# Performance work log

Hardware: AMD Instinct MI355X
Metric: run time of the kernel (lower is better)

## Reference

```python
import math
import jax, jax.numpy as jnp
import numpy as np

S, H, D = 2048, 16, 128

def setup_inputs() -> dict:
    key = jax.random.key(0)
    kq, kk, kv = jax.random.split(key, 3)
    Q = jax.random.normal(kq, (S, H, D), dtype=jnp.float32)
    K = jax.random.normal(kk, (S, H, D), dtype=jnp.float32)
    V = jax.random.normal(kv, (S, H, D), dtype=jnp.float32)
    return {"Q": Q, "K": K, "V": V}

def reference(Q, K, V):
    s, h, d = Q.shape
    # scores[i,h,j] = sum_d Q[i,h,d] * K[j,h,d]  (torch einsum 'ijk,kjl->ijl' with K.T)
    scores = jnp.einsum('ihd,jhd->ihj', Q, K) / np.float32(math.sqrt(d))
    # causal mask: y -= triu(inf, 1) broadcast over heads -> -inf above diagonal
    causal = jnp.triu(jnp.ones((s, s), dtype=bool), k=1)  # [S, S]
    scores = jnp.where(causal[:, None, :], -jnp.inf, scores)
    attn = jax.nn.softmax(scores, axis=2)  # softmax over keys (dim 2)
    # out[i,h,d] = sum_j attn[i,h,j] * V[j,h,d]
    return jnp.einsum('ihj,jhd->ihd', attn, V)
```

## Files before the change

### kernel.cpp

```cpp
#include <hip/hip_runtime.h>
#include <hip/hip_bf16.h>

#define S_LEN 2048
#define NH 16
#define HD 128
#define KBLK 128
#define SM_BOUND 14.0f

typedef short short8 __attribute__((ext_vector_type(8)));
typedef float f32x4 __attribute__((ext_vector_type(4)));

#define MFMA32(a, b, c) __builtin_amdgcn_mfma_f32_16x16x32_bf16(a, b, c, 0, 0, 0)

__device__ __forceinline__ ushort f2bf(float f) {
  union { float f; unsigned u; } v; v.f = f;
  unsigned u = v.u;
  return (ushort)((u + 0x7fffu + ((u >> 16) & 1u)) >> 16);
}

#define GLDS(gp, lp)                                                      \
  __builtin_amdgcn_global_load_lds(                                       \
      (const __attribute__((address_space(1))) void*)(gp),                \
      (__attribute__((address_space(3))) void*)(lp), 16, 0, 0)

__global__ __launch_bounds__(256)
void prep(const float* __restrict__ Kg, const float* __restrict__ Vg,
          ushort* __restrict__ Kb, ushort* __restrict__ Vb) {
  __shared__ ushort lt[64 * HD];
  const int tid = threadIdx.x;
  const int h = blockIdx.x & 15;
  const int j0 = (blockIdx.x >> 4) * 64;

#pragma unroll
  for (int it = 0; it < 8; ++it) {
    int flat = it * 256 + tid;
    int r = flat >> 5, d4 = (flat & 31) * 4;
    float4 v = *(const float4*)(Kg + ((size_t)(j0 + r) * NH + h) * HD + d4);
    ushort4 b;
    b.x = f2bf(v.x); b.y = f2bf(v.y); b.z = f2bf(v.z); b.w = f2bf(v.w);
    *(ushort4*)(Kb + ((size_t)h * S_LEN + j0 + r) * HD + d4) = b;
  }
#pragma unroll
  for (int it = 0; it < 8; ++it) {
    int flat = it * 256 + tid;
    int r = flat >> 5, d4 = (flat & 31) * 4;
    float4 v = *(const float4*)(Vg + ((size_t)(j0 + r) * NH + h) * HD + d4);
    ushort4 b;
    b.x = f2bf(v.x); b.y = f2bf(v.y); b.z = f2bf(v.z); b.w = f2bf(v.w);
    *(ushort4*)(&lt[r * 128 + (d4 ^ ((r & 7) << 3))]) = b;
  }
  __syncthreads();
  const int d = tid >> 1, half = tid & 1;
  ushort vals[32];
#pragma unroll
  for (int j = 0; j < 32; ++j) {
    int jjj = half * 32 + j;
    vals[j] = lt[jjj * 128 + (d ^ ((jjj & 7) << 3))];
  }
  ushort* dst = Vb + ((size_t)h * HD + d) * S_LEN + j0 + half * 32;
#pragma unroll
  for (int q = 0; q < 4; ++q) {
    short8 w;
#pragma unroll
    for (int e = 0; e < 8; ++e) w[e] = (short)vals[q * 8 + e];
    *(short8*)(dst + q * 8) = w;
  }
}

__global__ __launch_bounds__(512, 2)
void attn_fwd8(const float* __restrict__ Qg, const ushort* __restrict__ Kb,
               const ushort* __restrict__ Vb, float* __restrict__ Og) {
  __shared__ ushort lds_k[2][KBLK * HD];
  __shared__ ushort lds_vt[HD * KBLK];
  __shared__ ushort lds_p[64 * KBLK];
  __shared__ float  lsc[2][4][2][16];

  const int tid = threadIdx.x;
  const int l   = tid & 63;
  const int wv  = tid >> 6;
  const int qf  = wv >> 2;
  const int kh  = wv & 3;
  const int dh  = wv & 3;
  const int lr  = l & 15;
  const int lg  = l >> 4;

  const int bid = blockIdx.x;
  const int h   = bid & 15;
  const int jj  = bid >> 4;
  const int qtA = 31 - jj;
  const int qbA = qtA * 64, qbB = jj * 64;
  const int nchA = (qtA >> 1) + 1;
  const int nch  = 17;

  const ushort* khp = Kb + (size_t)h * S_LEN * HD;
  const ushort* vhp = Vb + (size_t)h * HD * S_LEN;

  int koff[4], voff[4];
#pragma unroll
  for (int i = 0; i < 4; ++i) {
    int Dg = i * 512 + tid;
    int r = Dg >> 4, gp = Dg & 15;
    koff[i] = r * 128 + ((gp ^ (r & 7)) << 3);
    voff[i] = r * S_LEN + ((gp ^ (r & 7)) << 3);
  }
  auto stageK = [&](int buf, int kc) {
    const ushort* kbase = khp + (size_t)kc * (KBLK * HD);
#pragma unroll
    for (int i = 0; i < 4; ++i)
      GLDS(kbase + koff[i], &lds_k[buf][(i * 512 + tid) * 8]);
  };
  auto stageV = [&](int kc) {
    const ushort* vbase = vhp + (size_t)kc * KBLK;
#pragma unroll
    for (int i = 0; i < 4; ++i)
      GLDS(vbase + voff[i], &lds_vt[(i * 512 + tid) * 8]);
  };
  auto kc_of = [&](int g) { return (g < nchA) ? g : (g - nchA); };

  const float scale = 0.08838834764831845f;
  short8 qfrA[2][4], qfrB[2][4];
  auto loadQ = [&](short8 (&dst)[2][4], int qb) {
#pragma unroll
    for (int qc = 0; qc < 2; ++qc) {
      const float* qsrc = Qg + ((size_t)(qb + qf * 32 + qc * 16 + lr) * NH + h) * HD;
#pragma unroll
      for (int dk = 0; dk < 4; ++dk) {
        float4 a = *(const float4*)(qsrc + dk * 32 + lg * 8);
        float4 b2 = *(const float4*)(qsrc + dk * 32 + lg * 8 + 4);
        short8 f;
        f[0] = (short)f2bf(a.x * scale);  f[1] = (short)f2bf(a.y * scale);
        f[2] = (short)f2bf(a.z * scale);  f[3] = (short)f2bf(a.w * scale);
        f[4] = (short)f2bf(b2.x * scale); f[5] = (short)f2bf(b2.y * scale);
        f[6] = (short)f2bf(b2.z * scale); f[7] = (short)f2bf(b2.w * scale);
        dst[qc][dk] = f;
      }
    }
  };
  loadQ(qfrA, qbA);
  loadQ(qfrB, qbB);

  f32x4 oacc[2][2];
#pragma unroll
  for (int qc = 0; qc < 2; ++qc)
#pragma unroll
    for (int dt = 0; dt < 2; ++dt) oacc[qc][dt] = (f32x4){0.f, 0.f, 0.f, 0.f};
  float l_run[2] = {0.f, 0.f};

  auto epilogue = [&](int qb) {
    float t0 = l_run[0], t1 = l_run[1];
    t0 += __shfl_xor(t0, 16, 64); t0 += __shfl_xor(t0, 32, 64);
    t1 += __shfl_xor(t1, 16, 64); t1 += __shfl_xor(t1, 32, 64);
    if (lg == 0) { lsc[qf][kh][0][lr] = t0; lsc[qf][kh][1][lr] = t1; }
    asm volatile("s_waitcnt lgkmcnt(0)" ::: "memory");
    asm volatile("s_barrier" ::: "memory");
    float inv[2][4];
#pragma unroll
    for (int qc = 0; qc < 2; ++qc)
#pragma unroll
      for (int i = 0; i < 4; ++i) {
        int q15 = lg * 4 + i;
        float sl = (lsc[qf][0][qc][q15] + lsc[qf][1][qc][q15]) +
                   (lsc[qf][2][qc][q15] + lsc[qf][3][qc][q15]);
        inv[qc][i] = 1.0f / sl;
      }
#pragma unroll
    for (int qc = 0; qc < 2; ++qc)
#pragma unroll
      for (int dt = 0; dt < 2; ++dt)
#pragma unroll
        for (int i = 0; i < 4; ++i) {
          int qg = qb + qf * 32 + qc * 16 + lg * 4 + i;
          Og[((size_t)qg * NH + h) * HD + dh * 32 + dt * 16 + lr] =
              oacc[qc][dt][i] * inv[qc][i];
        }
    asm volatile("s_barrier" ::: "memory");
  };

  stageK(0, 0);
  stageV(0);
  stageK(1, (nchA > 1) ? 1 : 0);
  asm volatile("s_waitcnt vmcnt(0)" ::: "memory");
  __syncthreads();

  for (int g = 0; g < nch; ++g) {
    if (g + 1 < nch) { asm volatile("s_waitcnt vmcnt(4)" ::: "memory"); }
    else             { asm volatile("s_waitcnt vmcnt(0)" ::: "memory"); }
    asm volatile("s_barrier" ::: "memory");

    const int b = g & 1;
    const ushort* lk = lds_k[b];
    const bool tB = (g >= nchA);
    const int kc = kc_of(g);
    const int qb = tB ? qbB : qbA;
    const bool diag = (g == nchA - 1) || (g == nch - 1);

    f32x4 s00 = (f32x4){0.f, 0.f, 0.f, 0.f};
    f32x4 s01 = (f32x4){0.f, 0.f, 0.f, 0.f};
    f32x4 s10 = (f32x4){0.f, 0.f, 0.f, 0.f};
    f32x4 s11 = (f32x4){0.f, 0.f, 0.f, 0.f};
    const int krow0 = kh * 32 + lr;
    const int krow1 = krow0 + 16;
    __builtin_amdgcn_s_setprio(1);
    if (!tB) {
#pragma unroll
      for (int dk = 0; dk < 4; ++dk) {
        short8 kf0 = *(const short8*)&lk[krow0 * 128 + ((dk * 32 + lg * 8) ^ ((krow0 & 7) << 3))];
        short8 kf1 = *(const short8*)&lk[krow1 * 128 + ((dk * 32 + lg * 8) ^ ((krow1 & 7) << 3))];
        s00 = MFMA32(kf0, qfrA[0][dk], s00);
        s01 = MFMA32(kf0, qfrA[1][dk], s01);
        s10 = MFMA32(kf1, qfrA[0][dk], s10);
        s11 = MFMA32(kf1, qfrA[1][dk], s11);
      }
    } else {
#pragma unroll
      for (int dk = 0; dk < 4; ++dk) {
        short8 kf0 = *(const short8*)&lk[krow0 * 128 + ((dk * 32 + lg * 8) ^ ((krow0 & 7) << 3))];
        short8 kf1 = *(const short8*)&lk[krow1 * 128 + ((dk * 32 + lg * 8) ^ ((krow1 & 7) << 3))];
        s00 = MFMA32(kf0, qfrB[0][dk], s00);
        s01 = MFMA32(kf0, qfrB[1][dk], s01);
        s10 = MFMA32(kf1, qfrB[0][dk], s10);
        s11 = MFMA32(kf1, qfrB[1][dk], s11);
      }
    }
    __builtin_amdgcn_s_setprio(0);

    float p[2][2][4];
    if (diag) {
#pragma unroll
      for (int qc = 0; qc < 2; ++qc) {
        int qg = qb + qf * 32 + qc * 16 + lr;
#pragma unroll
        for (int i = 0; i < 4; ++i) {
          int kg0 = kc * 128 + kh * 32 + lg * 4 + i;
          float e;
          e = __expf((qc ? s01 : s00)[i] - SM_BOUND);
          p[0][qc][i] = (kg0 > qg) ? 0.f : e;
          e = __expf((qc ? s11 : s10)[i] - SM_BOUND);
          p[1][qc][i] = (kg0 + 16 > qg) ? 0.f : e;
        }
      }
    } else {
#pragma unroll
      for (int i = 0; i < 4; ++i) {
        p[0][0][i] = __expf(s00[i] - SM_BOUND);
        p[0][1][i] = __expf(s01[i] - SM_BOUND);
        p[1][0][i] = __expf(s10[i] - SM_BOUND);
        p[1][1][i] = __expf(s11[i] - SM_BOUND);
      }
    }
#pragma unroll
    for (int qc = 0; qc < 2; ++qc)
      l_run[qc] += ((p[0][qc][0] + p[0][qc][1]) + (p[0][qc][2] + p[0][qc][3])) +
                   ((p[1][qc][0] + p[1][qc][1]) + (p[1][qc][2] + p[1][qc][3]));

#pragma unroll
    for (int qc = 0; qc < 2; ++qc) {
      int q = qf * 32 + qc * 16 + lr;
      int sw = (q & 7) << 3;
#pragma unroll
      for (int kcc = 0; kcc < 2; ++kcc) {
        int kb = kh * 32 + kcc * 16 + lg * 4;
        unsigned w;
        asm("v_cvt_pk_bf16_f32 %0, %1, %2" : "=v"(w) : "v"(p[kcc][qc][0]), "v"(p[kcc][qc][1]));
        *(unsigned*)&lds_p[q * 128 + ((((kb) >> 3 << 3) ^ sw) + (kb & 7))] = w;
        asm("v_cvt_pk_bf16_f32 %0, %1, %2" : "=v"(w) : "v"(p[kcc][qc][2]), "v"(p[kcc][qc][3]));
        *(unsigned*)&lds_p[q * 128 + ((((kb + 2) >> 3 << 3) ^ sw) + ((kb + 2) & 7))] = w;
      }
    }
    asm volatile("s_waitcnt lgkmcnt(0)" ::: "memory");
    asm volatile("s_barrier" ::: "memory");
    __builtin_amdgcn_sched_barrier(0);

    short8 pa0[4], pa1[4];
    {
      int q0 = qf * 32 + lr, q1 = q0 + 16;
#pragma unroll
      for (int ks = 0; ks < 4; ++ks) {
        pa0[ks] = *(const short8*)&lds_p[q0 * 128 + (((ks * 4 + lg) ^ (q0 & 7)) << 3)];
        pa1[ks] = *(const short8*)&lds_p[q1 * 128 + (((ks * 4 + lg) ^ (q1 & 7)) << 3)];
      }
    }
    __builtin_amdgcn_s_setprio(1);
#pragma unroll
    for (int dt = 0; dt < 2; ++dt) {
      int d = dh * 32 + dt * 16 + lr;
#pragma unroll
      for (int ks = 0; ks < 4; ++ks) {
        short8 vf = *(const short8*)&lds_vt[d * 128 + (((ks * 4 + lg) ^ (d & 7)) << 3)];
        oacc[0][dt] = MFMA32(pa0[ks], vf, oacc[0][dt]);
        oacc[1][dt] = MFMA32(pa1[ks], vf, oacc[1][dt]);
      }
    }
    __builtin_amdgcn_s_setprio(0);

    asm volatile("s_barrier" ::: "memory");
    if (g + 1 < nch) stageV(kc_of(g + 1));
    if (g + 2 < nch) stageK(b, kc_of(g + 2));

    if (g == nchA - 1) {
      epilogue(qbA);
#pragma unroll
      for (int qc = 0; qc < 2; ++qc)
#pragma unroll
        for (int dt = 0; dt < 2; ++dt) oacc[qc][dt] = (f32x4){0.f, 0.f, 0.f, 0.f};
      l_run[0] = 0.f; l_run[1] = 0.f;
    }
  }
  epilogue(qbB);
}

__global__ __launch_bounds__(256, 2)
void attn_fwd_fb(const float* __restrict__ Qg, const float* __restrict__ Kg,
                 const float* __restrict__ Vg, float* __restrict__ Og) {
  __shared__ ushort lds_k[64 * HD];
  __shared__ ushort lds_vt[HD * 64];
  __shared__ ushort lds_p[4][16 * 64];

  const int tid = threadIdx.x;
  const int l  = tid & 63;
  const int wv = tid >> 6;
  const int lr = l & 15;
  const int lg = l >> 4;

  const int bid = blockIdx.x;
  const int h  = bid & 15;
  const int qi = bid >> 4;
  const int qt = (qi < 16) ? (31 - 2 * qi) : (2 * (qi - 16));
  const int qbase = qt * 64;

  short8 qf[4];
  {
    const float* qsrc = Qg + ((size_t)(qbase + wv * 16 + lr) * NH + h) * HD;
#pragma unroll
    for (int dk = 0; dk < 4; ++dk) {
      float4 a = *(const float4*)(qsrc + dk * 32 + lg * 8);
      float4 b = *(const float4*)(qsrc + dk * 32 + lg * 8 + 4);
      short8 f;
      f[0] = (short)f2bf(a.x); f[1] = (short)f2bf(a.y);
      f[2] = (short)f2bf(a.z); f[3] = (short)f2bf(a.w);
      f[4] = (short)f2bf(b.x); f[5] = (short)f2bf(b.y);
      f[6] = (short)f2bf(b.z); f[7] = (short)f2bf(b.w);
      qf[dk] = f;
    }
  }

  f32x4 oacc[8];
#pragma unroll
  for (int dt = 0; dt < 8; ++dt) oacc[dt] = (f32x4){0.f, 0.f, 0.f, 0.f};
  float l_run[4] = {0.f, 0.f, 0.f, 0.f};

  const float scale = 0.08838834764831845f;
  const int nch = qt + 1;

  for (int c = 0; c < nch; ++c) {
    const int k0 = c * 64;
    __syncthreads();
#pragma unroll
    for (int it = 0; it < 8; ++it) {
      int flat = (it * 256 + tid) * 4;
      int r = flat >> 7, d = flat & 127;
      float4 v = *(const float4*)(Kg + ((size_t)(k0 + r) * NH + h) * HD + d);
      int idx = (r * 128 + d) ^ ((r & 7) << 3);
      ushort4 b4;
      b4.x = f2bf(v.x); b4.y = f2bf(v.y); b4.z = f2bf(v.z); b4.w = f2bf(v.w);
      *(ushort4*)&lds_k[idx] = b4;
    }
#pragma unroll
    for (int it = 0; it < 8; ++it) {
      int d0 = wv * 32 + it * 4;
      float4 v = *(const float4*)(Vg + ((size_t)(k0 + l) * NH + h) * HD + d0);
      lds_vt[((d0 + 0) * 64 + l) ^ (((d0 + 0) & 7) << 3)] = f2bf(v.x);
      lds_vt[((d0 + 1) * 64 + l) ^ (((d0 + 1) & 7) << 3)] = f2bf(v.y);
      lds_vt[((d0 + 2) * 64 + l) ^ (((d0 + 2) & 7) << 3)] = f2bf(v.z);
      lds_vt[((d0 + 3) * 64 + l) ^ (((d0 + 3) & 7) << 3)] = f2bf(v.w);
    }
    __syncthreads();

    f32x4 sacc[4];
#pragma unroll
    for (int kc = 0; kc < 4; ++kc) {
      sacc[kc] = (f32x4){0.f, 0.f, 0.f, 0.f};
#pragma unroll
      for (int dk = 0; dk < 4; ++dk) {
        int row = kc * 16 + lr;
        int idx = (row * 128 + dk * 32 + lg * 8) ^ ((row & 7) << 3);
        short8 kf = *(const short8*)&lds_k[idx];
        sacc[kc] = MFMA32(qf[dk], kf, sacc[kc]);
      }
    }

    float p[4][4];
    if (c == qt) {
#pragma unroll
      for (int i = 0; i < 4; ++i) {
        int qg = qbase + wv * 16 + lg * 4 + i;
#pragma unroll
        for (int kc = 0; kc < 4; ++kc) {
          float e = __expf(sacc[kc][i] * scale - SM_BOUND);
          p[kc][i] = (k0 + kc * 16 + lr > qg) ? 0.f : e;
        }
      }
    } else {
#pragma unroll
      for (int i = 0; i < 4; ++i)
#pragma unroll
        for (int kc = 0; kc < 4; ++kc)
          p[kc][i] = __expf(sacc[kc][i] * scale - SM_BOUND);
    }
#pragma unroll
    for (int i = 0; i < 4; ++i)
      l_run[i] += (p[0][i] + p[1][i]) + (p[2][i] + p[3][i]);

#pragma unroll
    for (int kc = 0; kc < 4; ++kc)
#pragma unroll
      for (int i = 0; i < 4; ++i) {
        int row = lg * 4 + i, col = kc * 16 + lr;
        lds_p[wv][(row * 64 + col) ^ ((row & 7) << 3)] = f2bf(p[kc][i]);
      }
    asm volatile("s_waitcnt lgkmcnt(0)" ::: "memory");
    __builtin_amdgcn_sched_barrier(0);

    short8 pa[2];
#pragma unroll
    for (int ks = 0; ks < 2; ++ks) {
      int idx = (lr * 64 + ks * 32 + lg * 8) ^ ((lr & 7) << 3);
      pa[ks] = *(const short8*)&lds_p[wv][idx];
    }

#pragma unroll
    for (int dt = 0; dt < 8; ++dt) {
#pragma unroll
      for (int ks = 0; ks < 2; ++ks) {
        int d = dt * 16 + lr;
        int idx = (d * 64 + ks * 32 + lg * 8) ^ ((d & 7) << 3);
        short8 vf = *(const short8*)&lds_vt[idx];
        oacc[dt] = MFMA32(pa[ks], vf, oacc[dt]);
      }
    }
  }

#pragma unroll
  for (int mk = 1; mk <= 8; mk <<= 1)
#pragma unroll
    for (int i = 0; i < 4; ++i)
      l_run[i] += __shfl_xor(l_run[i], mk, 64);
  float inv[4];
#pragma unroll
  for (int i = 0; i < 4; ++i) inv[i] = 1.0f / l_run[i];
#pragma unroll
  for (int dt = 0; dt < 8; ++dt)
#pragma unroll
    for (int i = 0; i < 4; ++i) {
      int qg = qbase + wv * 16 + lg * 4 + i;
      Og[((size_t)qg * NH + h) * HD + dt * 16 + lr] = oacc[dt][i] * inv[i];
    }
}

extern "C" void kernel_launch(void* const* d_in, const int* in_sizes, int n_in,
                              void* d_out, int out_size, void* d_ws, size_t ws_size,
                              hipStream_t stream) {
  (void)in_sizes; (void)n_in; (void)out_size;
  const float* Q = (const float*)d_in[0];
  const float* K = (const float*)d_in[1];
  const float* V = (const float*)d_in[2];
  float* O = (float*)d_out;

  const size_t elems = (size_t)S_LEN * NH * HD;
  const size_t need = 2 * elems * sizeof(ushort);
  if (ws_size >= need) {
    ushort* Kb = (ushort*)d_ws;
    ushort* Vb = Kb + elems;
    prep<<<dim3(512), dim3(256), 0, stream>>>(K, V, Kb, Vb);
    attn_fwd8<<<dim3(256), dim3(512), 0, stream>>>(Q, Kb, Vb, O);
  } else {
    attn_fwd_fb<<<dim3(512), dim3(256), 0, stream>>>(Q, K, V, O);
  }
}
```

Baseline: 60.14 us.

## Double workgroup size to 16 waves, halving per-wave key and head-dim slices

The attention kernel now runs 1024 threads (16 waves) per block instead of 512. Each wave handles 16 key rows of the S tile and 16 head-dim columns of the output rather than 32, so per-wave MFMA work, accumulator registers and staging loads are halved. The aim is more latency hiding and wave-level parallelism per CU with the same 256-block grid. In exchange, the 16 waves take part in every barrier, the row-sum reduction sums over 8 partials, and the launch bound of 4 blocks per CU may be unreachable given the LDS footprint.

New measurement: 127.4 us. 112% more time.

```diff
diff --git a/kernel.cpp b/kernel.cpp
--- a/kernel.cpp
+++ b/kernel.cpp
@@ -67,20 +67,20 @@
   }
 }
 
-__global__ __launch_bounds__(512, 2)
-void attn_fwd8(const float* __restrict__ Qg, const ushort* __restrict__ Kb,
+__global__ __launch_bounds__(1024, 4)
+void attn_fwd9(const float* __restrict__ Qg, const ushort* __restrict__ Kb,
                const ushort* __restrict__ Vb, float* __restrict__ Og) {
   __shared__ ushort lds_k[2][KBLK * HD];
   __shared__ ushort lds_vt[HD * KBLK];
   __shared__ ushort lds_p[64 * KBLK];
-  __shared__ float  lsc[2][4][2][16];
+  __shared__ float  lsc[2][8][2][16];
 
   const int tid = threadIdx.x;
   const int l   = tid & 63;
   const int wv  = tid >> 6;
-  const int qf  = wv >> 2;
-  const int kh  = wv & 3;
-  const int dh  = wv & 3;
+  const int qf  = wv >> 3;
+  const int kh  = wv & 7;
+  const int dh  = wv & 7;
   const int lr  = l & 15;
   const int lg  = l >> 4;
 
@@ -95,10 +95,10 @@
   const ushort* khp = Kb + (size_t)h * S_LEN * HD;
   const ushort* vhp = Vb + (size_t)h * HD * S_LEN;
 
-  int koff[4], voff[4];
-#pragma unroll
-  for (int i = 0; i < 4; ++i) {
-    int Dg = i * 512 + tid;
+  int koff[2], voff[2];
+#pragma unroll
+  for (int i = 0; i < 2; ++i) {
+    int Dg = i * 1024 + tid;
     int r = Dg >> 4, gp = Dg & 15;
     koff[i] = r * 128 + ((gp ^ (r & 7)) << 3);
     voff[i] = r * S_LEN + ((gp ^ (r & 7)) << 3);
@@ -106,14 +106,14 @@
   auto stageK = [&](int buf, int kc) {
     const ushort* kbase = khp + (size_t)kc * (KBLK * HD);
 #pragma unroll
-    for (int i = 0; i < 4; ++i)
-      GLDS(kbase + koff[i], &lds_k[buf][(i * 512 + tid) * 8]);
+    for (int i = 0; i < 2; ++i)
+      GLDS(kbase + koff[i], &lds_k[buf][(i * 1024 + tid) * 8]);
   };
   auto stageV = [&](int kc) {
     const ushort* vbase = vhp + (size_t)kc * KBLK;
 #pragma unroll
-    for (int i = 0; i < 4; ++i)
-      GLDS(vbase + voff[i], &lds_vt[(i * 512 + tid) * 8]);
+    for (int i = 0; i < 2; ++i)
+      GLDS(vbase + voff[i], &lds_vt[(i * 1024 + tid) * 8]);
   };
   auto kc_of = [&](int g) { return (g < nchA) ? g : (g - nchA); };
 
@@ -139,11 +139,9 @@
   loadQ(qfrA, qbA);
   loadQ(qfrB, qbB);
 
-  f32x4 oacc[2][2];
-#pragma unroll
-  for (int qc = 0; qc < 2; ++qc)
-#pragma unroll
-    for (int dt = 0; dt < 2; ++dt) oacc[qc][dt] = (f32x4){0.f, 0.f, 0.f, 0.f};
+  f32x4 oacc[2];
+  oacc[0] = (f32x4){0.f, 0.f, 0.f, 0.f};
+  oacc[1] = (f32x4){0.f, 0.f, 0.f, 0.f};
   float l_run[2] = {0.f, 0.f};
 
   auto epilogue = [&](int qb) {
@@ -159,31 +157,30 @@
 #pragma unroll
       for (int i = 0; i < 4; ++i) {
         int q15 = lg * 4 + i;
-        float sl = (lsc[qf][0][qc][q15] + lsc[qf][1][qc][q15]) +
-                   (lsc[qf][2][qc][q15] + lsc[qf][3][qc][q15]);
+        float sl = ((lsc[qf][0][qc][q15] + lsc[qf][1][qc][q15]) +
+                    (lsc[qf][2][qc][q15] + lsc[qf][3][qc][q15])) +
+                   ((lsc[qf][4][qc][q15] + lsc[qf][5][qc][q15]) +
+                    (lsc[qf][6][qc][q15] + lsc[qf][7][qc][q15]));
         inv[qc][i] = 1.0f / sl;
       }
 #pragma unroll
     for (int qc = 0; qc < 2; ++qc)
 #pragma unroll
-      for (int dt = 0; dt < 2; ++dt)
-#pragma unroll
-        for (int i = 0; i < 4; ++i) {
-          int qg = qb + qf * 32 + qc * 16 + lg * 4 + i;
-          Og[((size_t)qg * NH + h) * HD + dh * 32 + dt * 16 + lr] =
-              oacc[qc][dt][i] * inv[qc][i];
-        }
+      for (int i = 0; i < 4; ++i) {
+        int qg = qb + qf * 32 + qc * 16 + lg * 4 + i;
+        Og[((size_t)qg * NH + h) * HD + dh * 16 + lr] = oacc[qc][i] * inv[qc][i];
+      }
     asm volatile("s_barrier" ::: "memory");
   };
 
   stageK(0, 0);
   stageV(0);
-  stageK(1, (nchA > 1) ? 1 : 0);
+  stageK(1, 1);
   asm volatile("s_waitcnt vmcnt(0)" ::: "memory");
   __syncthreads();
 
   for (int g = 0; g < nch; ++g) {
-    if (g + 1 < nch) { asm volatile("s_waitcnt vmcnt(4)" ::: "memory"); }
+    if (g + 1 < nch) { asm volatile("s_waitcnt vmcnt(2)" ::: "memory"); }
     else             { asm volatile("s_waitcnt vmcnt(0)" ::: "memory"); }
     asm volatile("s_barrier" ::: "memory");
 
@@ -194,78 +191,59 @@
     const int qb = tB ? qbB : qbA;
     const bool diag = (g == nchA - 1) || (g == nch - 1);
 
-    f32x4 s00 = (f32x4){0.f, 0.f, 0.f, 0.f};
-    f32x4 s01 = (f32x4){0.f, 0.f, 0.f, 0.f};
-    f32x4 s10 = (f32x4){0.f, 0.f, 0.f, 0.f};
-    f32x4 s11 = (f32x4){0.f, 0.f, 0.f, 0.f};
-    const int krow0 = kh * 32 + lr;
-    const int krow1 = krow0 + 16;
+    f32x4 s0 = (f32x4){0.f, 0.f, 0.f, 0.f};
+    f32x4 s1 = (f32x4){0.f, 0.f, 0.f, 0.f};
+    const int krow = kh * 16 + lr;
     __builtin_amdgcn_s_setprio(1);
     if (!tB) {
 #pragma unroll
       for (int dk = 0; dk < 4; ++dk) {
-        short8 kf0 = *(const short8*)&lk[krow0 * 128 + ((dk * 32 + lg * 8) ^ ((krow0 & 7) << 3))];
-        short8 kf1 = *(const short8*)&lk[krow1 * 128 + ((dk * 32 + lg * 8) ^ ((krow1 & 7) << 3))];
-        s00 = MFMA32(kf0, qfrA[0][dk], s00);
-        s01 = MFMA32(kf0, qfrA[1][dk], s01);
-        s10 = MFMA32(kf1, qfrA[0][dk], s10);
-        s11 = MFMA32(kf1, qfrA[1][dk], s11);
+        short8 kf = *(const short8*)&lk[krow * 128 + ((dk * 32 + lg * 8) ^ ((krow & 7) << 3))];
+        s0 = MFMA32(kf, qfrA[0][dk], s0);
+        s1 = MFMA32(kf, qfrA[1][dk], s1);
       }
     } else {
 #pragma unroll
       for (int dk = 0; dk < 4; ++dk) {
-        short8 kf0 = *(const short8*)&lk[krow0 * 128 + ((dk * 32 + lg * 8) ^ ((krow0 & 7) << 3))];
-        short8 kf1 = *(const short8*)&lk[krow1 * 128 + ((dk * 32 + lg * 8) ^ ((krow1 & 7) << 3))];
-        s00 = MFMA32(kf0, qfrB[0][dk], s00);
-        s01 = MFMA32(kf0, qfrB[1][dk], s01);
-        s10 = MFMA32(kf1, qfrB[0][dk], s10);
-        s11 = MFMA32(kf1, qfrB[1][dk], s11);
+        short8 kf = *(const short8*)&lk[krow * 128 + ((dk * 32 + lg * 8) ^ ((krow & 7) << 3))];
+        s0 = MFMA32(kf, qfrB[0][dk], s0);
+        s1 = MFMA32(kf, qfrB[1][dk], s1);
       }
     }
     __builtin_amdgcn_s_setprio(0);
 
-    float p[2][2][4];
+    float p[2][4];
     if (diag) {
 #pragma unroll
       for (int qc = 0; qc < 2; ++qc) {
         int qg = qb + qf * 32 + qc * 16 + lr;
 #pragma unroll
         for (int i = 0; i < 4; ++i) {
-          int kg0 = kc * 128 + kh * 32 + lg * 4 + i;
-          float e;
-          e = __expf((qc ? s01 : s00)[i] - SM_BOUND);
-          p[0][qc][i] = (kg0 > qg) ? 0.f : e;
-          e = __expf((qc ? s11 : s10)[i] - SM_BOUND);
-          p[1][qc][i] = (kg0 + 16 > qg) ? 0.f : e;
+          int kg = kc * 128 + kh * 16 + lg * 4 + i;
+          float e = __expf((qc ? s1 : s0)[i] - SM_BOUND);
+          p[qc][i] = (kg > qg) ? 0.f : e;
         }
       }
     } else {
 #pragma unroll
       for (int i = 0; i < 4; ++i) {
-        p[0][0][i] = __expf(s00[i] - SM_BOUND);
-        p[0][1][i] = __expf(s01[i] - SM_BOUND);
-        p[1][0][i] = __expf(s10[i] - SM_BOUND);
-        p[1][1][i] = __expf(s11[i] - SM_BOUND);
-      }
-    }
-#pragma unroll
-    for (int qc = 0; qc < 2; ++qc)
-      l_run[qc] += ((p[0][qc][0] + p[0][qc][1]) + (p[0][qc][2] + p[0][qc][3])) +
-                   ((p[1][qc][0] + p[1][qc][1]) + (p[1][qc][2] + p[1][qc][3]));
+        p[0][i] = __expf(s0[i] - SM_BOUND);
+        p[1][i] = __expf(s1[i] - SM_BOUND);
+      }
+    }
+    l_run[0] += (p[0][0] + p[0][1]) + (p[0][2] + p[0][3]);
+    l_run[1] += (p[1][0] + p[1][1]) + (p[1][2] + p[1][3]);
 
 #pragma unroll
     for (int qc = 0; qc < 2; ++qc) {
       int q = qf * 32 + qc * 16 + lr;
       int sw = (q & 7) << 3;
-#pragma unroll
-      for (int kcc = 0; kcc < 2; ++kcc) {
-        int kb = kh * 32 + kcc * 16 + lg * 4;
-        unsigned w;
-        asm("v_cvt_pk_bf16_f32 %0, %1, %2" : "=v"(w) : "v"(p[kcc][qc][0]), "v"(p[kcc][qc][1]));
-        *(unsigned*)&lds_p[q * 128 + ((((kb) >> 3 << 3) ^ sw) + (kb & 7))] = w;
-        asm("v_cvt_pk_bf16_f32 %0, %1, %2" : "=v"(w) : "v"(p[kcc][qc][2]), "v"(p[kcc][qc][3]));
-        *(unsigned*)&lds_p[q * 128 + ((((kb + 2) >> 3 << 3) ^ sw) + ((kb + 2) & 7))] = w;
-      }
+      int kb = kh * 16 + lg * 4;
+      unsigned w;
+      asm("v_cvt_pk_bf16_f32 %0, %1, %2" : "=v"(w) : "v"(p[qc][0]), "v"(p[qc][1]));
+      *(unsigned*)&lds_p[q * 128 + (((kb >> 3 << 3) ^ sw) + (kb & 7))] = w;
+      asm("v_cvt_pk_bf16_f32 %0, %1, %2" : "=v"(w) : "v"(p[qc][2]), "v"(p[qc][3]));
+      *(unsigned*)&lds_p[q * 128 + ((((kb + 2) >> 3 << 3) ^ sw) + ((kb + 2) & 7))] = w;
     }
     asm volatile("s_waitcnt lgkmcnt(0)" ::: "memory");
     asm volatile("s_barrier" ::: "memory");
@@ -281,14 +259,13 @@
       }
     }
     __builtin_amdgcn_s_setprio(1);
-#pragma unroll
-    for (int dt = 0; dt < 2; ++dt) {
-      int d = dh * 32 + dt * 16 + lr;
+    {
+      int d = dh * 16 + lr;
 #pragma unroll
       for (int ks = 0; ks < 4; ++ks) {
         short8 vf = *(const short8*)&lds_vt[d * 128 + (((ks * 4 + lg) ^ (d & 7)) << 3)];
-        oacc[0][dt] = MFMA32(pa0[ks], vf, oacc[0][dt]);
-        oacc[1][dt] = MFMA32(pa1[ks], vf, oacc[1][dt]);
+        oacc[0] = MFMA32(pa0[ks], vf, oacc[0]);
+        oacc[1] = MFMA32(pa1[ks], vf, oacc[1]);
       }
     }
     __builtin_amdgcn_s_setprio(0);
@@ -299,10 +276,8 @@
 
     if (g == nchA - 1) {
       epilogue(qbA);
-#pragma unroll
-      for (int qc = 0; qc < 2; ++qc)
-#pragma unroll
-        for (int dt = 0; dt < 2; ++dt) oacc[qc][dt] = (f32x4){0.f, 0.f, 0.f, 0.f};
+      oacc[0] = (f32x4){0.f, 0.f, 0.f, 0.f};
+      oacc[1] = (f32x4){0.f, 0.f, 0.f, 0.f};
       l_run[0] = 0.f; l_run[1] = 0.f;
     }
   }
@@ -472,7 +447,7 @@
     ushort* Kb = (ushort*)d_ws;
     ushort* Vb = Kb + elems;
     prep<<<dim3(512), dim3(256), 0, stream>>>(K, V, Kb, Vb);
-    attn_fwd8<<<dim3(256), dim3(512), 0, stream>>>(Q, Kb, Vb, O);
+    attn_fwd9<<<dim3(256), dim3(1024), 0, stream>>>(Q, Kb, Vb, O);
   } else {
     attn_fwd_fb<<<dim3(512), dim3(256), 0, stream>>>(Q, K, V, O);
   }
```
